# Optimization experiments

Measured on AMD Instinct MI355X. Metric: run time of the kernel, lower is better.

## Reference

```python
import jax, jax.numpy as jnp
import numpy as np

B, T, U, H, M, K, C = 64, 800, 80, 512, 20, 10, 80  # batch, tsteps, char len, rnn_size, nmixtures, kmixtures, char_vec_len


def _lstm(x, W, Uw, b):
    """Keras-semantics LSTM (gate order i,f,g,o), zero initial state. x: [B,T,D] -> [B,T,H]."""
    xg = jnp.einsum('btd,dh->bth', x, W) + b  # precompute input contribution
    h0 = jnp.zeros((x.shape[0], Uw.shape[0]), x.dtype)
    c0 = jnp.zeros_like(h0)

    def step(carry, zt):
        h, c = carry
        z = zt + h @ Uw
        i, f, g, o = jnp.split(z, 4, axis=-1)
        c = jax.nn.sigmoid(f) * c + jax.nn.sigmoid(i) * jnp.tanh(g)
        h = jax.nn.sigmoid(o) * jnp.tanh(c)
        return (h, c), h

    _, hs = jax.lax.scan(step, (h0, c0), jnp.swapaxes(xg, 0, 1))
    return jnp.swapaxes(hs, 0, 1)


def _forward(stroke_data, char_seq, kappa0, W0, U0, b0, W1, U1, b1, W2, U2, b2, Wa, ba, Wm, bm):
    lstm0_out = _lstm(stroke_data, W0, U0, b0)  # [B,T,H]
    # Attention window: the per-timestep loop in the source only carries kappa,
    # which is a running sum of exp(kappa_offset) -> vectorize via cumsum.
    abk = jnp.exp(jnp.einsum('bth,hk->btk', lstm0_out, Wa) + ba)  # [B,T,3K]
    alpha, beta, koff = jnpp_split = jnp.split(abk, 3, axis=-1)
    kappa = kappa0[:, None, :, 0] + jnp.cumsum(koff, axis=1)  # [B,T,K]
    u = jnp.arange(char_seq.shape[1], dtype=stroke_data.dtype)  # [U]
    # phi: [B,T,U] = sum_k alpha * exp(-beta * (kappa - u)^2)
    phi = jnp.sum(alpha[..., None] * jnp.exp(-beta[..., None] * (kappa[..., None] - u) ** 2), axis=2)
    windows = jnp.einsum('btu,buc->btc', phi, char_seq)  # [B,T,C]
    aug = jnp.concatenate([lstm0_out, windows, stroke_data], axis=-1)
    lstm1_out = _lstm(aug, W1, U1, b1)
    lstm2_out = _lstm(lstm1_out, W2, U2, b2)
    mdn = jnp.einsum('bth,hn->btn', lstm2_out, Wm) + bm  # [B,T,1+6M]
    eos_hat = mdn[..., 0:1]
    pi_hat, mu1, mu2, s1_hat, s2_hat, rho_hat = jnp.split(mdn[..., 1:], 6, axis=-1)
    return jnp.concatenate([
        jax.nn.sigmoid(-eos_hat),
        jax.nn.softmax(pi_hat, axis=-1),
        mu1, mu2,
        jnp.exp(s1_hat), jnp.exp(s2_hat),
        jnp.tanh(rho_hat),
    ], axis=-1)  # [B,T,1+6M]


def setup_inputs() -> dict:
    key = jax.random.key(0)
    ks = jax.random.split(key, 12)
    init = lambda k, shape: jax.random.truncated_normal(k, -2.0, 2.0, shape, jnp.float32) * 0.075
    return {
        'stroke_data': jax.random.normal(ks[0], (B, T, 3), jnp.float32),
        'char_seq': jax.nn.one_hot(jax.random.randint(ks[1], (B, U), 0, C), C, dtype=jnp.float32),
        'kappa0': jnp.zeros((B, K, 1), jnp.float32),
        'W0': init(ks[2], (3, 4 * H)), 'U0': init(ks[3], (H, 4 * H)), 'b0': jnp.zeros((4 * H,)),
        'W1': init(ks[4], (H + C + 3, 4 * H)), 'U1': init(ks[5], (H, 4 * H)), 'b1': jnp.zeros((4 * H,)),
        'W2': init(ks[6], (H, 4 * H)), 'U2': init(ks[7], (H, 4 * H)), 'b2': jnp.zeros((4 * H,)),
        'Wa': init(ks[8], (H, 3 * K)),
        'ba': -3.0 + 0.25 * jax.random.truncated_normal(ks[9], -2.0, 2.0, (3 * K,), jnp.float32),
        'Wm': init(ks[10], (H, 1 + 6 * M)), 'bm': jnp.zeros((1 + 6 * M,)),
    }


def reference(stroke_data, char_seq, kappa0, W0, U0, b0, W1, U1, b1, W2, U2, b2, Wa, ba, Wm, bm):
    return _forward(stroke_data, char_seq, kappa0, W0, U0, b0, W1, U1, b1, W2, U2, b2, Wa, ba, Wm, bm)
```

## Files before the change

kernel.cpp:

```cpp
#include <hip/hip_runtime.h>

typedef unsigned short u16;
typedef unsigned int u32;
typedef short v8s __attribute__((ext_vector_type(8)));
typedef float v4f __attribute__((ext_vector_type(4)));
typedef unsigned int v4u __attribute__((ext_vector_type(4)));
typedef unsigned int v2u __attribute__((ext_vector_type(2)));

#define MFMA16 __builtin_amdgcn_mfma_f32_16x16x32_bf16

constexpr int TT = 800;
constexpr int NBLK = 184;
constexpr int GRP = 23;

constexpr int AUGB  = 2240;
constexpr int AUG2B = 2048;

constexpr size_t AUGR_OFF  = 8192;
constexpr size_t AUG2R_OFF = AUGR_OFF + (size_t)4 * 64 * AUGB;
constexpr size_t WAT_OFF   = AUG2R_OFF + (size_t)4 * 64 * AUG2B;
constexpr size_t WS_ZERO   = WAT_OFF + (size_t)32 * 512 * 2;

__device__ __forceinline__ float bf2f(u16 u) { return __uint_as_float(((u32)u) << 16); }
__device__ __forceinline__ u16 f2bf(float f) {
    u32 x = __float_as_uint(f);
    return (u16)((x + 0x7fffu + ((x >> 16) & 1u)) >> 16);
}
__device__ __forceinline__ short f2bfs(float f) { return (short)f2bf(f); }
__device__ __forceinline__ float sigf(float x) { return 1.f / (1.f + __expf(-x)); }
__device__ __forceinline__ float tanhf2(float x) { return 1.f - 2.f / (1.f + __expf(2.f * x)); }

__device__ __forceinline__ __amdgpu_buffer_rsrc_t mkrsrc(const void* p) {
    return __builtin_amdgcn_make_buffer_rsrc((void*)p, (short)0, -1, 0x00020000);
}
__device__ __forceinline__ v4u ldu4(__amdgpu_buffer_rsrc_t r, int off) {
    return __builtin_amdgcn_raw_buffer_load_b128(r, off, 0, 17);
}
__device__ __forceinline__ void stq8(__amdgpu_buffer_rsrc_t r, int off, u16 a, u16 b, u16 c, u16 d) {
    v2u t; t[0] = (u32)a | ((u32)b << 16); t[1] = (u32)c | ((u32)d << 16);
    __builtin_amdgcn_raw_buffer_store_b64(t, r, off, 0, 17);
}
__device__ __forceinline__ void stq4(__amdgpu_buffer_rsrc_t r, int off, u16 a, u16 b) {
    u32 t = (u32)a | ((u32)b << 16);
    __builtin_amdgcn_raw_buffer_store_b32(t, r, off, 0, 17);
}

__device__ __forceinline__ void gbar(u32* ctrl, u32 target) {
    __syncthreads();
    if (threadIdx.x == 0) {
        const int g = blockIdx.x & 7;
        u32* cnt = ctrl + g * 64;
        u32* sup = ctrl + 512;
        u32* gen = ctrl + 576 + g * 64;
        bool released = false;
        u32 old = __hip_atomic_fetch_add(cnt, 1u, __ATOMIC_RELAXED, __HIP_MEMORY_SCOPE_AGENT);
        if (old == target * GRP - 1) {
            u32 so = __hip_atomic_fetch_add(sup, 1u, __ATOMIC_RELAXED, __HIP_MEMORY_SCOPE_AGENT);
            if (so == target * 8 - 1) {
                #pragma unroll
                for (int k = 0; k < 8; k++)
                    __hip_atomic_store(ctrl + 576 + k * 64, target, __ATOMIC_RELAXED, __HIP_MEMORY_SCOPE_AGENT);
                released = true;
            }
        }
        if (!released) {
            while (__hip_atomic_load(gen, __ATOMIC_RELAXED, __HIP_MEMORY_SCOPE_AGENT) < target)
                __builtin_amdgcn_s_sleep(8);
        }
    }
    __syncthreads();
}

__global__ void wat_init(const float* __restrict__ Wa, u16* __restrict__ WaT) {
    __amdgpu_buffer_rsrc_t r = mkrsrc(WaT);
    for (int idx = blockIdx.x * 256 + threadIdx.x; idx < 32 * 512 / 2; idx += gridDim.x * 256) {
        const int e0 = idx * 2, e1 = e0 + 1;
        const int n0 = e0 >> 9, k0 = e0 & 511;
        const int n1 = e1 >> 9, k1 = e1 & 511;
        const u16 a = (n0 < 30) ? f2bf(Wa[k0 * 30 + n0]) : (u16)0;
        const u16 b = (n1 < 30) ? f2bf(Wa[k1 * 30 + n1]) : (u16)0;
        stq4(r, idx * 4, a, b);
    }
}

__global__ __launch_bounds__(256, 1) void hw_main(
    const float* __restrict__ stroke, const float* __restrict__ charseq, const float* __restrict__ kappa0,
    const float* __restrict__ W0, const float* __restrict__ U0, const float* __restrict__ b0,
    const float* __restrict__ W1, const float* __restrict__ U1, const float* __restrict__ b1,
    const float* __restrict__ W2, const float* __restrict__ U2, const float* __restrict__ b2,
    const float* __restrict__ ba, const float* __restrict__ Wm, const float* __restrict__ bm,
    float* __restrict__ out, char* __restrict__ ws)
{
    __shared__ __align__(16) char smem[55296];
    u32* ctrl = (u32*)ws;
    u16* augr  = (u16*)(ws + AUGR_OFF);
    u16* aug2r = (u16*)(ws + AUG2R_OFF);
    const u16* WaT = (const u16*)(ws + WAT_OFF);

    const int blk = blockIdx.x, tid = threadIdx.x;
    const int wave = tid >> 6, lane = tid & 63;
    const int quad = lane >> 4, l15 = lane & 15;

    if (blk < 32) {
        const int cs = blk & 15, mg = blk >> 4;
        __amdgpu_buffer_rsrc_t ra = mkrsrc(augr);
        u16*   aL  = (u16*)smem;
        float* zb  = (float*)(smem + 33280);
        float* w0s = (float*)(smem + 50176);
        float* b0s = (float*)(smem + 51712);
        if (tid < 128) {
            const int cn2 = (tid >> 5) * 512 + cs * 32 + (tid & 31);
            b0s[tid] = b0[cn2];
            #pragma unroll
            for (int d = 0; d < 3; d++) w0s[d * 128 + tid] = W0[d * 2048 + cn2];
        }
        v8s bw0[16], bw1[16];
        {
            const int cnA = wave * 512 + cs * 32 + l15;
            const int cnB = cnA + 16;
            #pragma unroll
            for (int kc = 0; kc < 16; kc++)
                #pragma unroll
                for (int j = 0; j < 8; j++) {
                    const int k = kc * 32 + quad * 8 + j;
                    bw0[kc][j] = f2bfs(U0[k * 2048 + cnA]);
                    bw1[kc][j] = f2bfs(U0[k * 2048 + cnB]);
                }
        }
        float cst[4] = {0.f, 0.f, 0.f, 0.f};
        __syncthreads();
        #pragma unroll 1
        for (int i = 0; i <= TT + 3; i++) {
            if (i < TT) {
                const int t = i;
                {
                    const int base = (((t + 3) & 3) * 64 + mg * 32) * AUGB;
                    #pragma unroll
                    for (int c8 = 0; c8 < 8; c8++) {
                        const int c = tid + 256 * c8;
                        const int row = c >> 6, off = c & 63;
                        v4u d = ldu4(ra, base + row * AUGB + off * 16);
                        *(v4u*)((char*)aL + row * 1040 + off * 16) = d;
                    }
                }
                __syncthreads();
                v4f c0a = {0,0,0,0}, c0b = {0,0,0,0}, c1a = {0,0,0,0}, c1b = {0,0,0,0};
                const int xo = quad * 16;
                #pragma unroll
                for (int kc = 0; kc < 16; kc++) {
                    v8s x0 = *(const v8s*)((const char*)aL + l15 * 1040 + kc * 64 + xo);
                    v8s x1 = *(const v8s*)((const char*)aL + (16 + l15) * 1040 + kc * 64 + xo);
                    c0a = MFMA16(x0, bw0[kc], c0a, 0, 0, 0);
                    c1a = MFMA16(x0, bw1[kc], c1a, 0, 0, 0);
                    c0b = MFMA16(x1, bw0[kc], c0b, 0, 0, 0);
                    c1b = MFMA16(x1, bw1[kc], c1b, 0, 0, 0);
                }
                const int n0 = wave * 32 + l15, n1 = n0 + 16;
                #pragma unroll
                for (int r = 0; r < 4; r++) {
                    zb[(quad * 4 + r) * 132 + n0] = c0a[r];
                    zb[(quad * 4 + r) * 132 + n1] = c1a[r];
                    zb[(16 + quad * 4 + r) * 132 + n0] = c0b[r];
                    zb[(16 + quad * 4 + r) * 132 + n1] = c1b[r];
                }
                __syncthreads();
                {
                    const int bl = tid & 31, jj = tid >> 5;
                    const int b = mg * 32 + bl;
                    const float xx0 = stroke[(b * TT + t) * 3 + 0];
                    const float xx1 = stroke[(b * TT + t) * 3 + 1];
                    const float xx2 = stroke[(b * TT + t) * 3 + 2];
                    u16 hv[4];
                    #pragma unroll
                    for (int m = 0; m < 4; m++) {
                        const int j = jj * 4 + m;
                        float z[4];
                        #pragma unroll
                        for (int g = 0; g < 4; g++) {
                            const int n = g * 32 + j;
                            z[g] = zb[bl * 132 + n] + b0s[n] + xx0 * w0s[n] + xx1 * w0s[128 + n] + xx2 * w0s[256 + n];
                        }
                        const float cc = sigf(z[1]) * cst[m] + sigf(z[0]) * tanhf2(z[2]);
                        cst[m] = cc;
                        hv[m] = f2bf(sigf(z[3]) * tanhf2(cc));
                    }
                    stq8(ra, ((t & 3) * 64 + b) * AUGB + (cs * 32 + jj * 4) * 2, hv[0], hv[1], hv[2], hv[3]);
                }
            }
            if (i < TT + 3) gbar(ctrl, (u32)(i + 1));
        }
    } else if (blk < 96) {
        const int q = blk - 32, cs = q & 15, mg = q >> 4;
        __amdgpu_buffer_rsrc_t ra = mkrsrc(augr);
        __amdgpu_buffer_rsrc_t r2 = mkrsrc(aug2r);
        u16*   aL  = (u16*)smem;
        float* zb  = (float*)(smem + 36096);
        float* b1s = (float*)(smem + 44544);
        if (tid < 128) b1s[tid] = b1[(tid >> 5) * 512 + cs * 32 + (tid & 31)];
        v8s bw0[35], bw1[35];
        {
            const int cnA = wave * 512 + cs * 32 + l15;
            const int cnB = cnA + 16;
            #pragma unroll
            for (int kc = 0; kc < 35; kc++)
                #pragma unroll
                for (int j = 0; j < 8; j++) {
                    const int k = kc * 32 + quad * 8 + j;
                    short vA = 0, vB = 0;
                    if (k < 595) { vA = f2bfs(W1[k * 2048 + cnA]); vB = f2bfs(W1[k * 2048 + cnB]); }
                    else if (k >= 596 && k < 1108) { vA = f2bfs(U1[(k - 596) * 2048 + cnA]); vB = f2bfs(U1[(k - 596) * 2048 + cnB]); }
                    bw0[kc][j] = vA; bw1[kc][j] = vB;
                }
        }
        float cst[2] = {0.f, 0.f};
        __syncthreads();
        #pragma unroll 1
        for (int i = 0; i <= TT + 3; i++) {
            if (i >= 2 && i <= TT + 1) {
                const int t1 = i - 2;
                {
                    const int base = ((t1 & 3) * 64 + mg * 16) * AUGB;
                    #pragma unroll
                    for (int c9 = 0; c9 < 9; c9++) {
                        const int c = tid + 256 * c9;
                        if (c < 2240) {
                            const int row = c / 140, off = c - row * 140;
                            v4u d = ldu4(ra, base + row * AUGB + off * 16);
                            *(v4u*)((char*)aL + row * 2256 + off * 16) = d;
                        }
                    }
                }
                __syncthreads();
                v4f c0 = {0,0,0,0}, c1 = {0,0,0,0};
                const int xo = quad * 16;
                #pragma unroll
                for (int kc = 0; kc < 35; kc++) {
                    v8s x = *(const v8s*)((const char*)aL + l15 * 2256 + kc * 64 + xo);
                    c0 = MFMA16(x, bw0[kc], c0, 0, 0, 0);
                    c1 = MFMA16(x, bw1[kc], c1, 0, 0, 0);
                }
                const int n0 = wave * 32 + l15, n1 = n0 + 16;
                #pragma unroll
                for (int r = 0; r < 4; r++) {
                    zb[(quad * 4 + r) * 132 + n0] = c0[r];
                    zb[(quad * 4 + r) * 132 + n1] = c1[r];
                }
                __syncthreads();
                {
                    const int bl = tid & 15, jj = tid >> 4;
                    const int b = mg * 16 + bl;
                    u16 hv[2];
                    #pragma unroll
                    for (int m = 0; m < 2; m++) {
                        const int j = jj * 2 + m;
                        float z[4];
                        #pragma unroll
                        for (int g = 0; g < 4; g++)
                            z[g] = zb[bl * 132 + g * 32 + j] + b1s[g * 32 + j];
                        const float cc = sigf(z[1]) * cst[m] + sigf(z[0]) * tanhf2(z[2]);
                        cst[m] = cc;
                        hv[m] = f2bf(sigf(z[3]) * tanhf2(cc));
                    }
                    stq4(ra, (((t1 + 1) & 3) * 64 + b) * AUGB + (596 + cs * 32 + jj * 2) * 2, hv[0], hv[1]);
                    stq4(r2, ((t1 & 3) * 64 + b) * AUG2B + (cs * 32 + jj * 2) * 2, hv[0], hv[1]);
                }
            }
            if (i < TT + 3) gbar(ctrl, (u32)(i + 1));
        }
    } else if (blk < 160) {
        const int q = blk - 96, cs = q & 15, mg = q >> 4;
        __amdgpu_buffer_rsrc_t r2 = mkrsrc(aug2r);
        u16*   aL  = (u16*)smem;
        float* zb  = (float*)(smem + 33024);
        float* b2s = (float*)(smem + 41472);
        if (tid < 128) b2s[tid] = b2[(tid >> 5) * 512 + cs * 32 + (tid & 31)];
        v8s bw0[32], bw1[32];
        {
            const int cnA = wave * 512 + cs * 32 + l15;
            const int cnB = cnA + 16;
            #pragma unroll
            for (int kc = 0; kc < 32; kc++)
                #pragma unroll
                for (int j = 0; j < 8; j++) {
                    const int k = kc * 32 + quad * 8 + j;
                    bw0[kc][j] = (k < 512) ? f2bfs(W2[k * 2048 + cnA]) : f2bfs(U2[(k - 512) * 2048 + cnA]);
                    bw1[kc][j] = (k < 512) ? f2bfs(W2[k * 2048 + cnB]) : f2bfs(U2[(k - 512) * 2048 + cnB]);
                }
        }
        float cst[2] = {0.f, 0.f};
        __syncthreads();
        #pragma unroll 1
        for (int i = 0; i <= TT + 3; i++) {
            if (i >= 3 && i <= TT + 2) {
                const int t2 = i - 3;
                {
                    const int base = ((t2 & 3) * 64 + mg * 16) * AUG2B;
                    #pragma unroll
                    for (int c8 = 0; c8 < 8; c8++) {
                        const int c = tid + 256 * c8;
                        const int row = c >> 7, off = c & 127;
                        v4u d = ldu4(r2, base + row * AUG2B + off * 16);
                        *(v4u*)((char*)aL + row * 2064 + off * 16) = d;
                    }
                }
                __syncthreads();
                v4f c0 = {0,0,0,0}, c1 = {0,0,0,0};
                const int xo = quad * 16;
                #pragma unroll
                for (int kc = 0; kc < 32; kc++) {
                    v8s x = *(const v8s*)((const char*)aL + l15 * 2064 + kc * 64 + xo);
                    c0 = MFMA16(x, bw0[kc], c0, 0, 0, 0);
                    c1 = MFMA16(x, bw1[kc], c1, 0, 0, 0);
                }
                const int n0 = wave * 32 + l15, n1 = n0 + 16;
                #pragma unroll
                for (int r = 0; r < 4; r++) {
                    zb[(quad * 4 + r) * 132 + n0] = c0[r];
                    zb[(quad * 4 + r) * 132 + n1] = c1[r];
                }
                __syncthreads();
                {
                    const int bl = tid & 15, jj = tid >> 4;
                    const int b = mg * 16 + bl;
                    u16 hv[2];
                    #pragma unroll
                    for (int m = 0; m < 2; m++) {
                        const int j = jj * 2 + m;
                        float z[4];
                        #pragma unroll
                        for (int g = 0; g < 4; g++)
                            z[g] = zb[bl * 132 + g * 32 + j] + b2s[g * 32 + j];
                        const float cc = sigf(z[1]) * cst[m] + sigf(z[0]) * tanhf2(z[2]);
                        cst[m] = cc;
                        hv[m] = f2bf(sigf(z[3]) * tanhf2(cc));
                    }
                    stq4(r2, (((t2 + 1) & 3) * 64 + b) * AUG2B + (512 + cs * 32 + jj * 2) * 2, hv[0], hv[1]);
                }
            }
            if (i < TT + 3) gbar(ctrl, (u32)(i + 1));
        }
    } else if (blk < 176) {
        const int a = blk - 160;
        const int b = a * 4 + wave;
        __amdgpu_buffer_rsrc_t ra = mkrsrc(augr);
        u16*   watl = (u16*)smem;
        u16*   hrow = (u16*)(smem + 33280);
        float* phis = (float*)(smem + 37440);
        u16*   idxs = (u16*)(smem + 38720);
        {
            #pragma unroll
            for (int c8 = 0; c8 < 8; c8++) {
                const int c = tid + 256 * c8;
                const int row = c >> 6, off = c & 63;
                *(v4u*)((char*)watl + row * 1040 + off * 16) = *(const v4u*)(WaT + row * 512 + off * 8);
            }
        }
        #pragma unroll
        for (int rep = 0; rep < 2; rep++) {
            const int u = rep * 64 + lane;
            if (u < 80) {
                int c = 0;
                #pragma unroll 1
                for (int cc = 0; cc < 80; cc++)
                    if (charseq[b * 6400 + u * 80 + cc] > 0.5f) c = cc;
                idxs[wave * 80 + u] = (u16)c;
            }
        }
        float kap = (lane < 10) ? kappa0[b * 10 + lane] : 0.f;
        const float baf = (lane < 30) ? ba[lane] : 0.f;
        const int nn = lane & 31;
        const int k0 = (lane >> 5) * 256;
        const u16* wrow = watl + nn * 520 + k0;
        __syncthreads();
        #pragma unroll 1
        for (int i = 0; i <= TT + 3; i++) {
            if (i >= 1 && i <= TT) {
                const int ta = i - 1;
                {
                    const int row = tid >> 6, off = tid & 63;
                    v4u d = ldu4(ra, ((ta & 3) * 64 + a * 4 + row) * AUGB + off * 16);
                    *(v4u*)((char*)hrow + row * 1040 + off * 16) = d;
                }
                __syncthreads();
                float acc = 0.f;
                #pragma unroll
                for (int kk = 0; kk < 32; kk++) {
                    v8s hv = *(const v8s*)((const char*)hrow + wave * 1040 + (k0 + kk * 8) * 2);
                    v8s wv = *(const v8s*)(wrow + kk * 8);
                    #pragma unroll
                    for (int e = 0; e < 8; e++) acc += bf2f((u16)hv[e]) * bf2f((u16)wv[e]);
                }
                acc += __shfl_xor(acc, 32);
                const float abk = __expf(acc + baf);
                const float kofv = __shfl(abk, 20 + (lane < 10 ? lane : 0));
                if (lane < 10) kap += kofv;
                const float u1f = (float)lane, u2f = (float)(64 + lane);
                float p1 = 0.f, p2 = 0.f;
                #pragma unroll
                for (int kk = 0; kk < 10; kk++) {
                    const float al = __shfl(abk, kk);
                    const float be = __shfl(abk, 10 + kk);
                    const float kp = __shfl(kap, kk);
                    const float d1 = kp - u1f, d2 = kp - u2f;
                    p1 += al * __expf(-be * d1 * d1);
                    p2 += al * __expf(-be * d2 * d2);
                }
                phis[wave * 80 + lane] = p1;
                if (lane < 16) phis[wave * 80 + 64 + lane] = p2;
                __syncthreads();
                const int db = (((ta & 3) * 64 + b) * AUGB) + 512 * 2;
                if (lane < 40) {
                    const int c0 = 2 * lane;
                    float w0 = 0.f, w1 = 0.f;
                    #pragma unroll 1
                    for (int u = 0; u < 80; u++) {
                        const float pv = phis[wave * 80 + u];
                        const int ix = (int)idxs[wave * 80 + u];
                        w0 += (ix == c0)     ? pv : 0.f;
                        w1 += (ix == c0 + 1) ? pv : 0.f;
                    }
                    stq4(ra, db + c0 * 2, f2bf(w0), f2bf(w1));
                } else if (lane == 40) {
                    stq4(ra, db + 80 * 2, f2bf(stroke[(b * TT + ta) * 3 + 0]), f2bf(stroke[(b * TT + ta) * 3 + 1]));
                } else if (lane == 41) {
                    stq4(ra, db + 82 * 2, f2bf(stroke[(b * TT + ta) * 3 + 2]), (u16)0);
                }
            }
            if (i < TT + 3) gbar(ctrl, (u32)(i + 1));
        }
    } else if (blk < 178) {
        const int mgs = blk - 176;
        __amdgpu_buffer_rsrc_t r2 = mkrsrc(aug2r);
        u16*   aL = (u16*)smem;
        float* zb = (float*)(smem + 33280);
        v8s bw0[16], bw1[16];
        {
            const int nA = wave * 32 + l15, nB = nA + 16;
            #pragma unroll
            for (int kc = 0; kc < 16; kc++)
                #pragma unroll
                for (int j = 0; j < 8; j++) {
                    const int k = kc * 32 + quad * 8 + j;
                    bw0[kc][j] = (nA < 121) ? f2bfs(Wm[k * 121 + nA]) : (short)0;
                    bw1[kc][j] = (nB < 121) ? f2bfs(Wm[k * 121 + nB]) : (short)0;
                }
        }
        __syncthreads();
        #pragma unroll 1
        for (int i = 0; i <= TT + 3; i++) {
            if (i >= 4) {
                const int tm = i - 4;
                {
                    const int base = (((tm + 1) & 3) * 64 + mgs * 32) * AUG2B + 1024;
                    #pragma unroll
                    for (int c8 = 0; c8 < 8; c8++) {
                        const int c = tid + 256 * c8;
                        const int row = c >> 6, off = c & 63;
                        v4u d = ldu4(r2, base + row * AUG2B + off * 16);
                        *(v4u*)((char*)aL + row * 1040 + off * 16) = d;
                    }
                }
                __syncthreads();
                v4f c0a = {0,0,0,0}, c0b = {0,0,0,0}, c1a = {0,0,0,0}, c1b = {0,0,0,0};
                const int xo = quad * 16;
                #pragma unroll
                for (int kc = 0; kc < 16; kc++) {
                    v8s x0 = *(const v8s*)((const char*)aL + l15 * 1040 + kc * 64 + xo);
                    v8s x1 = *(const v8s*)((const char*)aL + (16 + l15) * 1040 + kc * 64 + xo);
                    c0a = MFMA16(x0, bw0[kc], c0a, 0, 0, 0);
                    c1a = MFMA16(x0, bw1[kc], c1a, 0, 0, 0);
                    c0b = MFMA16(x1, bw0[kc], c0b, 0, 0, 0);
                    c1b = MFMA16(x1, bw1[kc], c1b, 0, 0, 0);
                }
                const int n0 = wave * 32 + l15, n1 = n0 + 16;
                #pragma unroll
                for (int r = 0; r < 4; r++) {
                    zb[(quad * 4 + r) * 132 + n0] = c0a[r];
                    zb[(quad * 4 + r) * 132 + n1] = c1a[r];
                    zb[(16 + quad * 4 + r) * 132 + n0] = c0b[r];
                    zb[(16 + quad * 4 + r) * 132 + n1] = c1b[r];
                }
                __syncthreads();
                {
                    const int b8 = tid >> 3, g8 = tid & 7;
                    const int b = mgs * 32 + b8;
                    const float* zr = zb + b8 * 132;
                    float* orow = out + ((size_t)(b * TT + tm)) * 121;
                    if (g8 == 0) {
                        orow[0] = sigf(-(zr[0] + bm[0]));
                        float mx = -1e30f;
                        float zv[20];
                        #pragma unroll 1
                        for (int nl = 1; nl <= 20; nl++) { zv[nl - 1] = zr[nl] + bm[nl]; mx = fmaxf(mx, zv[nl - 1]); }
                        float ss = 0.f;
                        #pragma unroll 1
                        for (int nl = 0; nl < 20; nl++) { zv[nl] = __expf(zv[nl] - mx); ss += zv[nl]; }
                        const float inv = 1.f / ss;
                        #pragma unroll 1
                        for (int nl = 0; nl < 20; nl++) orow[nl + 1] = zv[nl] * inv;
                    } else if (g8 <= 2) {
                        const int s0 = 21 + (g8 - 1) * 20;
                        #pragma unroll 1
                        for (int nl = s0; nl < s0 + 20; nl++) orow[nl] = zr[nl] + bm[nl];
                    } else if (g8 <= 4) {
                        const int s0 = 61 + (g8 - 3) * 20;
                        #pragma unroll 1
                        for (int nl = s0; nl < s0 + 20; nl++) orow[nl] = __expf(zr[nl] + bm[nl]);
                    } else if (g8 <= 6) {
                        const int s0 = 101 + (g8 - 5) * 10;
                        #pragma unroll 1
                        for (int nl = s0; nl < s0 + 10; nl++) orow[nl] = tanhf2(zr[nl] + bm[nl]);
                    }
                }
            }
            if (i < TT + 3) gbar(ctrl, (u32)(i + 1));
        }
    } else {
        #pragma unroll 1
        for (int i = 0; i <= TT + 3; i++)
            if (i < TT + 3) gbar(ctrl, (u32)(i + 1));
    }
}

extern "C" void kernel_launch(void* const* d_in, const int* in_sizes, int n_in,
                              void* d_out, int out_size, void* d_ws, size_t ws_size,
                              hipStream_t stream) {
    const float* stroke  = (const float*)d_in[0];
    const float* charseq = (const float*)d_in[1];
    const float* kappa0  = (const float*)d_in[2];
    const float* W0 = (const float*)d_in[3];
    const float* U0 = (const float*)d_in[4];
    const float* b0 = (const float*)d_in[5];
    const float* W1 = (const float*)d_in[6];
    const float* U1 = (const float*)d_in[7];
    const float* b1 = (const float*)d_in[8];
    const float* W2 = (const float*)d_in[9];
    const float* U2 = (const float*)d_in[10];
    const float* b2 = (const float*)d_in[11];
    const float* Wa = (const float*)d_in[12];
    const float* ba = (const float*)d_in[13];
    const float* Wm = (const float*)d_in[14];
    const float* bm = (const float*)d_in[15];
    char* ws = (char*)d_ws;

    hipMemsetAsync(d_ws, 0, WS_ZERO, stream);
    wat_init<<<8, 256, 0, stream>>>(Wa, (u16*)(ws + WAT_OFF));
    hw_main<<<NBLK, 256, 0, stream>>>(stroke, charseq, kappa0, W0, U0, b0,
                                      W1, U1, b1, W2, U2, b2, ba, Wm, bm,
                                      (float*)d_out, ws);
}
```

Baseline: 9.628 ms.

## Retile LSTM1/2 blocks to 16 columns by 32 batch rows, flatten grid barrier

The LSTM1 and LSTM2 blocks now each own 16 hidden columns across 32 batch rows instead of 32 columns across 16 rows. Each block holds half the weight registers and reuses each weight fragment for two MFMAs over two batch halves. This needs twice the activation staging in shared memory, so the kernel moves to 82944 bytes of dynamic shared memory. The hierarchical grouped grid barrier is replaced by one flat atomic counter that releases 32 generation words, with a short-then-longer sleep spin. The idle filler blocks are dropped, cutting the grid from 184 to 178 blocks. The trade-off is more contention on the single counter and per-step staging of twice as many activation rows.

Measured after the change: 10.46 ms. 1.09x slower.

```diff
diff --git a/kernel.cpp b/kernel.cpp
--- a/kernel.cpp
+++ b/kernel.cpp
@@ -10,16 +10,17 @@
 #define MFMA16 __builtin_amdgcn_mfma_f32_16x16x32_bf16
 
 constexpr int TT = 800;
-constexpr int NBLK = 184;
-constexpr int GRP = 23;
+constexpr int NBLK = 178;
 
 constexpr int AUGB  = 2240;
 constexpr int AUG2B = 2048;
 
-constexpr size_t AUGR_OFF  = 8192;
+constexpr size_t AUGR_OFF  = 16384;
 constexpr size_t AUG2R_OFF = AUGR_OFF + (size_t)4 * 64 * AUGB;
 constexpr size_t WAT_OFF   = AUG2R_OFF + (size_t)4 * 64 * AUG2B;
 constexpr size_t WS_ZERO   = WAT_OFF + (size_t)32 * 512 * 2;
+
+constexpr u32 SMEM_BYTES = 82944;
 
 __device__ __forceinline__ float bf2f(u16 u) { return __uint_as_float(((u32)u) << 16); }
 __device__ __forceinline__ u16 f2bf(float f) {
@@ -48,24 +49,19 @@
 __device__ __forceinline__ void gbar(u32* ctrl, u32 target) {
     __syncthreads();
     if (threadIdx.x == 0) {
-        const int g = blockIdx.x & 7;
-        u32* cnt = ctrl + g * 64;
-        u32* sup = ctrl + 512;
-        u32* gen = ctrl + 576 + g * 64;
-        bool released = false;
-        u32 old = __hip_atomic_fetch_add(cnt, 1u, __ATOMIC_RELAXED, __HIP_MEMORY_SCOPE_AGENT);
-        if (old == target * GRP - 1) {
-            u32 so = __hip_atomic_fetch_add(sup, 1u, __ATOMIC_RELAXED, __HIP_MEMORY_SCOPE_AGENT);
-            if (so == target * 8 - 1) {
-                #pragma unroll
-                for (int k = 0; k < 8; k++)
-                    __hip_atomic_store(ctrl + 576 + k * 64, target, __ATOMIC_RELAXED, __HIP_MEMORY_SCOPE_AGENT);
-                released = true;
-            }
-        }
-        if (!released) {
-            while (__hip_atomic_load(gen, __ATOMIC_RELAXED, __HIP_MEMORY_SCOPE_AGENT) < target)
-                __builtin_amdgcn_s_sleep(8);
+        u32 old = __hip_atomic_fetch_add(ctrl, 1u, __ATOMIC_RELAXED, __HIP_MEMORY_SCOPE_AGENT);
+        if (old == target * NBLK - 1) {
+            #pragma unroll
+            for (int k = 0; k < 32; k++)
+                __hip_atomic_store(ctrl + 1024 + k * 64, target, __ATOMIC_RELAXED, __HIP_MEMORY_SCOPE_AGENT);
+        } else {
+            u32* gen = ctrl + 1024 + (blockIdx.x & 31) * 64;
+            int sp = 0;
+            while (__hip_atomic_load(gen, __ATOMIC_RELAXED, __HIP_MEMORY_SCOPE_AGENT) < target) {
+                if (sp >= 2) __builtin_amdgcn_s_sleep(8);
+                else if (sp == 1) __builtin_amdgcn_s_sleep(1);
+                sp++;
+            }
         }
     }
     __syncthreads();
@@ -91,7 +87,7 @@
     const float* __restrict__ ba, const float* __restrict__ Wm, const float* __restrict__ bm,
     float* __restrict__ out, char* __restrict__ ws)
 {
-    __shared__ __align__(16) char smem[55296];
+    extern __shared__ __align__(16) char smem[];
     u32* ctrl = (u32*)ws;
     u16* augr  = (u16*)(ws + AUGR_OFF);
     u16* aug2r = (u16*)(ws + AUG2R_OFF);
@@ -190,26 +186,25 @@
             if (i < TT + 3) gbar(ctrl, (u32)(i + 1));
         }
     } else if (blk < 96) {
-        const int q = blk - 32, cs = q & 15, mg = q >> 4;
+        const int q = blk - 32, cs = q >> 1, mg = q & 1;
         __amdgpu_buffer_rsrc_t ra = mkrsrc(augr);
         __amdgpu_buffer_rsrc_t r2 = mkrsrc(aug2r);
         u16*   aL  = (u16*)smem;
-        float* zb  = (float*)(smem + 36096);
-        float* b1s = (float*)(smem + 44544);
-        if (tid < 128) b1s[tid] = b1[(tid >> 5) * 512 + cs * 32 + (tid & 31)];
-        v8s bw0[35], bw1[35];
+        float* zb  = (float*)(smem + 72192);
+        float* b1s = (float*)(smem + 80896);
+        if (tid < 64) b1s[tid] = b1[(tid >> 4) * 512 + cs * 16 + (tid & 15)];
+        v8s bw[35];
         {
-            const int cnA = wave * 512 + cs * 32 + l15;
-            const int cnB = cnA + 16;
+            const int cn = wave * 512 + cs * 16 + l15;
             #pragma unroll
             for (int kc = 0; kc < 35; kc++)
                 #pragma unroll
                 for (int j = 0; j < 8; j++) {
                     const int k = kc * 32 + quad * 8 + j;
-                    short vA = 0, vB = 0;
-                    if (k < 595) { vA = f2bfs(W1[k * 2048 + cnA]); vB = f2bfs(W1[k * 2048 + cnB]); }
-                    else if (k >= 596 && k < 1108) { vA = f2bfs(U1[(k - 596) * 2048 + cnA]); vB = f2bfs(U1[(k - 596) * 2048 + cnB]); }
-                    bw0[kc][j] = vA; bw1[kc][j] = vB;
+                    short v = 0;
+                    if (k < 595) v = f2bfs(W1[k * 2048 + cn]);
+                    else if (k >= 596 && k < 1108) v = f2bfs(U1[(k - 596) * 2048 + cn]);
+                    bw[kc][j] = v;
                 }
         }
         float cst[2] = {0.f, 0.f};
@@ -219,11 +214,11 @@
             if (i >= 2 && i <= TT + 1) {
                 const int t1 = i - 2;
                 {
-                    const int base = ((t1 & 3) * 64 + mg * 16) * AUGB;
-                    #pragma unroll
-                    for (int c9 = 0; c9 < 9; c9++) {
-                        const int c = tid + 256 * c9;
-                        if (c < 2240) {
+                    const int base = ((t1 & 3) * 64 + mg * 32) * AUGB;
+                    #pragma unroll
+                    for (int c18 = 0; c18 < 18; c18++) {
+                        const int c = tid + 256 * c18;
+                        if (c < 4480) {
                             const int row = c / 140, off = c - row * 140;
                             v4u d = ldu4(ra, base + row * AUGB + off * 16);
                             *(v4u*)((char*)aL + row * 2256 + off * 16) = d;
@@ -235,20 +230,20 @@
                 const int xo = quad * 16;
                 #pragma unroll
                 for (int kc = 0; kc < 35; kc++) {
-                    v8s x = *(const v8s*)((const char*)aL + l15 * 2256 + kc * 64 + xo);
-                    c0 = MFMA16(x, bw0[kc], c0, 0, 0, 0);
-                    c1 = MFMA16(x, bw1[kc], c1, 0, 0, 0);
-                }
-                const int n0 = wave * 32 + l15, n1 = n0 + 16;
+                    v8s x0 = *(const v8s*)((const char*)aL + l15 * 2256 + kc * 64 + xo);
+                    v8s x1 = *(const v8s*)((const char*)aL + (16 + l15) * 2256 + kc * 64 + xo);
+                    c0 = MFMA16(x0, bw[kc], c0, 0, 0, 0);
+                    c1 = MFMA16(x1, bw[kc], c1, 0, 0, 0);
+                }
                 #pragma unroll
                 for (int r = 0; r < 4; r++) {
-                    zb[(quad * 4 + r) * 132 + n0] = c0[r];
-                    zb[(quad * 4 + r) * 132 + n1] = c1[r];
-                }
-                __syncthreads();
-                {
-                    const int bl = tid & 15, jj = tid >> 4;
-                    const int b = mg * 16 + bl;
+                    zb[(quad * 4 + r) * 68 + wave * 17 + l15] = c0[r];
+                    zb[(16 + quad * 4 + r) * 68 + wave * 17 + l15] = c1[r];
+                }
+                __syncthreads();
+                {
+                    const int bl = tid & 31, jj = tid >> 5;
+                    const int b = mg * 32 + bl;
                     u16 hv[2];
                     #pragma unroll
                     for (int m = 0; m < 2; m++) {
@@ -256,35 +251,33 @@
                         float z[4];
                         #pragma unroll
                         for (int g = 0; g < 4; g++)
-                            z[g] = zb[bl * 132 + g * 32 + j] + b1s[g * 32 + j];
+                            z[g] = zb[bl * 68 + g * 17 + j] + b1s[g * 16 + j];
                         const float cc = sigf(z[1]) * cst[m] + sigf(z[0]) * tanhf2(z[2]);
                         cst[m] = cc;
                         hv[m] = f2bf(sigf(z[3]) * tanhf2(cc));
                     }
-                    stq4(ra, (((t1 + 1) & 3) * 64 + b) * AUGB + (596 + cs * 32 + jj * 2) * 2, hv[0], hv[1]);
-                    stq4(r2, ((t1 & 3) * 64 + b) * AUG2B + (cs * 32 + jj * 2) * 2, hv[0], hv[1]);
+                    stq4(ra, (((t1 + 1) & 3) * 64 + b) * AUGB + (596 + cs * 16 + jj * 2) * 2, hv[0], hv[1]);
+                    stq4(r2, ((t1 & 3) * 64 + b) * AUG2B + (cs * 16 + jj * 2) * 2, hv[0], hv[1]);
                 }
             }
             if (i < TT + 3) gbar(ctrl, (u32)(i + 1));
         }
     } else if (blk < 160) {
-        const int q = blk - 96, cs = q & 15, mg = q >> 4;
+        const int q = blk - 96, cs = q >> 1, mg = q & 1;
         __amdgpu_buffer_rsrc_t r2 = mkrsrc(aug2r);
         u16*   aL  = (u16*)smem;
-        float* zb  = (float*)(smem + 33024);
-        float* b2s = (float*)(smem + 41472);
-        if (tid < 128) b2s[tid] = b2[(tid >> 5) * 512 + cs * 32 + (tid & 31)];
-        v8s bw0[32], bw1[32];
+        float* zb  = (float*)(smem + 66048);
+        float* b2s = (float*)(smem + 74752);
+        if (tid < 64) b2s[tid] = b2[(tid >> 4) * 512 + cs * 16 + (tid & 15)];
+        v8s bw[32];
         {
-            const int cnA = wave * 512 + cs * 32 + l15;
-            const int cnB = cnA + 16;
+            const int cn = wave * 512 + cs * 16 + l15;
             #pragma unroll
             for (int kc = 0; kc < 32; kc++)
                 #pragma unroll
                 for (int j = 0; j < 8; j++) {
                     const int k = kc * 32 + quad * 8 + j;
-                    bw0[kc][j] = (k < 512) ? f2bfs(W2[k * 2048 + cnA]) : f2bfs(U2[(k - 512) * 2048 + cnA]);
-                    bw1[kc][j] = (k < 512) ? f2bfs(W2[k * 2048 + cnB]) : f2bfs(U2[(k - 512) * 2048 + cnB]);
+                    bw[kc][j] = (k < 512) ? f2bfs(W2[k * 2048 + cn]) : f2bfs(U2[(k - 512) * 2048 + cn]);
                 }
         }
         float cst[2] = {0.f, 0.f};
@@ -294,10 +287,10 @@
             if (i >= 3 && i <= TT + 2) {
                 const int t2 = i - 3;
                 {
-                    const int base = ((t2 & 3) * 64 + mg * 16) * AUG2B;
-                    #pragma unroll
-                    for (int c8 = 0; c8 < 8; c8++) {
-                        const int c = tid + 256 * c8;
+                    const int base = ((t2 & 3) * 64 + mg * 32) * AUG2B;
+                    #pragma unroll
+                    for (int c16 = 0; c16 < 16; c16++) {
+                        const int c = tid + 256 * c16;
                         const int row = c >> 7, off = c & 127;
                         v4u d = ldu4(r2, base + row * AUG2B + off * 16);
                         *(v4u*)((char*)aL + row * 2064 + off * 16) = d;
@@ -308,20 +301,20 @@
                 const int xo = quad * 16;
                 #pragma unroll
                 for (int kc = 0; kc < 32; kc++) {
-                    v8s x = *(const v8s*)((const char*)aL + l15 * 2064 + kc * 64 + xo);
-                    c0 = MFMA16(x, bw0[kc], c0, 0, 0, 0);
-                    c1 = MFMA16(x, bw1[kc], c1, 0, 0, 0);
-                }
-                const int n0 = wave * 32 + l15, n1 = n0 + 16;
+                    v8s x0 = *(const v8s*)((const char*)aL + l15 * 2064 + kc * 64 + xo);
+                    v8s x1 = *(const v8s*)((const char*)aL + (16 + l15) * 2064 + kc * 64 + xo);
+                    c0 = MFMA16(x0, bw[kc], c0, 0, 0, 0);
+                    c1 = MFMA16(x1, bw[kc], c1, 0, 0, 0);
+                }
                 #pragma unroll
                 for (int r = 0; r < 4; r++) {
-                    zb[(quad * 4 + r) * 132 + n0] = c0[r];
-                    zb[(quad * 4 + r) * 132 + n1] = c1[r];
-                }
-                __syncthreads();
-                {
-                    const int bl = tid & 15, jj = tid >> 4;
-                    const int b = mg * 16 + bl;
+                    zb[(quad * 4 + r) * 68 + wave * 17 + l15] = c0[r];
+                    zb[(16 + quad * 4 + r) * 68 + wave * 17 + l15] = c1[r];
+                }
+                __syncthreads();
+                {
+                    const int bl = tid & 31, jj = tid >> 5;
+                    const int b = mg * 32 + bl;
                     u16 hv[2];
                     #pragma unroll
                     for (int m = 0; m < 2; m++) {
@@ -329,12 +322,12 @@
                         float z[4];
                         #pragma unroll
                         for (int g = 0; g < 4; g++)
-                            z[g] = zb[bl * 132 + g * 32 + j] + b2s[g * 32 + j];
+                            z[g] = zb[bl * 68 + g * 17 + j] + b2s[g * 16 + j];
                         const float cc = sigf(z[1]) * cst[m] + sigf(z[0]) * tanhf2(z[2]);
                         cst[m] = cc;
                         hv[m] = f2bf(sigf(z[3]) * tanhf2(cc));
                     }
-                    stq4(r2, (((t2 + 1) & 3) * 64 + b) * AUG2B + (512 + cs * 32 + jj * 2) * 2, hv[0], hv[1]);
+                    stq4(r2, (((t2 + 1) & 3) * 64 + b) * AUG2B + (512 + cs * 16 + jj * 2) * 2, hv[0], hv[1]);
                 }
             }
             if (i < TT + 3) gbar(ctrl, (u32)(i + 1));
@@ -515,10 +508,6 @@
             }
             if (i < TT + 3) gbar(ctrl, (u32)(i + 1));
         }
-    } else {
-        #pragma unroll 1
-        for (int i = 0; i <= TT + 3; i++)
-            if (i < TT + 3) gbar(ctrl, (u32)(i + 1));
     }
 }
 
@@ -543,9 +532,16 @@
     const float* bm = (const float*)d_in[15];
     char* ws = (char*)d_ws;
 
+    static bool attr_done = false;
+    if (!attr_done) {
+        hipFuncSetAttribute((const void*)hw_main,
+                            hipFuncAttributeMaxDynamicSharedMemorySize, SMEM_BYTES);
+        attr_done = true;
+    }
+
     hipMemsetAsync(d_ws, 0, WS_ZERO, stream);
     wat_init<<<8, 256, 0, stream>>>(Wa, (u16*)(ws + WAT_OFF));
-    hw_main<<<NBLK, 256, 0, stream>>>(stroke, charseq, kappa0, W0, U0, b0,
-                                      W1, U1, b1, W2, U2, b2, ba, Wm, bm,
-                                      (float*)d_out, ws);
-}
+    hw_main<<<NBLK, 256, SMEM_BYTES, stream>>>(stroke, charseq, kappa0, W0, U0, b0,
+                                               W1, U1, b1, W2, U2, b2, ba, Wm, bm,
+                                               (float*)d_out, ws);
+}
```
